# Kernel optimization log

Measured on AMD Instinct MI355X. Metric: run time of the kernel, lower is better.

The kernel has to match this reference:

```python
import jax, jax.numpy as jnp
import numpy as np

# ArcFace hyperparameters (match init_kwargs)
M1 = 1.0
M2 = 0.5
M3 = 0.0
SCALE = 64.0
LS = 0.0  # label_smoothing
THRESHOLD = float(np.cos((np.pi - M2) / M1))  # easy-margin threshold
THETA_MIN = (-1.0 - M3) * 2.0

B, C = 512, 100000


def setup_inputs() -> dict:
    key = jax.random.key(0)
    kl, kx = jax.random.split(key)
    labels = jax.random.randint(kl, (B,), 0, C)
    # y_true is a one-hot target matrix, as implied by `torch.where(y_true != 0)` picking one entry per row
    y_true = jax.nn.one_hot(labels, C, dtype=jnp.float32)
    # norm_logits are cosine similarities in (-1, 1); keep away from endpoints so acos is well-conditioned
    norm_logits = jax.random.uniform(kx, (B, C), jnp.float32, -0.99, 0.99)
    return {"y_true": y_true, "norm_logits": norm_logits}


def reference(y_true, norm_logits):
    b, c = norm_logits.shape
    labels = jnp.argmax(y_true, axis=-1)           # [B] index of the single nonzero per row
    rows = jnp.arange(b)
    vals = norm_logits[rows, labels]               # gather cos(theta) at true-label positions
    # margin1 == 1.0 and margin3 == 0.0 -> theta = cos(acos(x) + m2) branch
    theta = jnp.cos(jnp.arccos(vals) * M1 + M2) - M3
    theta_valid = jnp.where(vals > THRESHOLD, theta, THETA_MIN - theta)
    arcface_logits = norm_logits.at[rows, labels].set(theta_valid) * SCALE
    log_p = jax.nn.log_softmax(arcface_logits, axis=-1)
    # F.cross_entropy with probability targets + label smoothing
    target = y_true * (1.0 - LS) + LS / c
    return -jnp.mean(jnp.sum(target * log_p, axis=-1))
```

## Files before the change

kernel.cpp:

```cpp
#include <hip/hip_runtime.h>
#include <math.h>


#define BB 512
#define CC 100000
#define C4 (CC / 4)
#define BLK 1024

#define K64 92.33248261689366f

typedef unsigned int u32x4 __attribute__((ext_vector_type(4)));
typedef float f32x4 __attribute__((ext_vector_type(4)));

__device__ __forceinline__ float wave_reduce_add(float v) {
    #pragma unroll
    for (int off = 32; off > 0; off >>= 1)
        v += __shfl_down(v, off, 64);
    return v;
}

__device__ __forceinline__ float e64(float x) {
    return __builtin_amdgcn_exp2f(fmaf(K64, x, -K64));
}

__global__ __launch_bounds__(BLK) void arcface_rows(const float* __restrict__ y_true,
                                                    const float* __restrict__ logits,
                                                    float* __restrict__ row_loss) {
    const int row = blockIdx.x;
    const int tid = threadIdx.x;
    const u32x4* __restrict__ y4 = (const u32x4*)(y_true + (size_t)row * CC);
    const f32x4* __restrict__ x4 = (const f32x4*)(logits + (size_t)row * CC);

    __shared__ int s_lab;
    __shared__ float s_sum[BLK / 64];

    #pragma unroll 1
    for (int i = tid; i < C4; i += BLK) {
        const u32x4 u = __builtin_nontemporal_load(&y4[i]);
        if (u.x | u.y | u.z | u.w) {
            const int off = u.x ? 0 : (u.y ? 1 : (u.z ? 2 : 3));
            s_lab = 4 * i + off;
        }
    }
    __syncthreads();

    float val = 0.0f;
    if (tid == 0) val = logits[(size_t)row * CC + s_lab];

    float s0 = 0.0f, s1 = 0.0f;
    #pragma unroll 1
    for (int i = tid; i < C4; i += BLK) {
        const f32x4 x = x4[i];
        s0 += e64(x.x); s1 += e64(x.y); s0 += e64(x.z); s1 += e64(x.w);
    }

    float s = wave_reduce_add(s0 + s1);
    if ((tid & 63) == 0) s_sum[tid >> 6] = s;
    __syncthreads();

    if (tid == 0) {
        float total = 0.0f;
        #pragma unroll
        for (int w = 0; w < BLK / 64; ++w) total += s_sum[w];

        const float THRESH = -0.8775825618903728f;
        const float theta = cosf(acosf(val) + 0.5f);
        const float tv = (val > THRESH) ? theta : (-2.0f - theta);

        total += e64(tv) - e64(val);

        row_loss[row] = 64.0f + logf(total) - 64.0f * tv;
    }
}

__global__ __launch_bounds__(BB) void reduce_rows(const float* __restrict__ row_loss,
                                                  float* __restrict__ out) {
    const int tid = threadIdx.x;
    float v = row_loss[tid];
    v = wave_reduce_add(v);
    __shared__ float s_wave[BB / 64];
    if ((tid & 63) == 0) s_wave[tid >> 6] = v;
    __syncthreads();
    if (tid == 0) {
        float t = 0.0f;
        #pragma unroll
        for (int w = 0; w < BB / 64; ++w) t += s_wave[w];
        out[0] = t * (1.0f / (float)BB);
    }
}

extern "C" void kernel_launch(void* const* d_in, const int* in_sizes, int n_in,
                              void* d_out, int out_size, void* d_ws, size_t ws_size,
                              hipStream_t stream) {
    const float* y_true = (const float*)d_in[0];
    const float* logits = (const float*)d_in[1];
    float* out = (float*)d_out;
    float* row_loss = (float*)d_ws;

    arcface_rows<<<BB, BLK, 0, stream>>>(y_true, logits, row_loss);
    reduce_rows<<<1, BB, 0, stream>>>(row_loss, out);
}
```

Before: 64.30 us.

## Stop one-hot scan early and fuse final mean via atomicAdd

Threads scanning a row of the one-hot matrix now check a shared volatile flag and stop as soon as any thread in the block has found the label, which skips the remaining y_true reads for that row. The separate reduction kernel is replaced by a memset of the output plus an atomicAdd of each row's scaled loss. The early exit only helps when the label lies early in a thread's stride, because every thread still reads its first chunk. The atomic accumulation makes the summation order nondeterministic.

```diff
diff --git a/kernel.cpp b/kernel.cpp
--- a/kernel.cpp
+++ b/kernel.cpp
@@ -25,7 +25,7 @@
 
 __global__ __launch_bounds__(BLK) void arcface_rows(const float* __restrict__ y_true,
                                                     const float* __restrict__ logits,
-                                                    float* __restrict__ row_loss) {
+                                                    float* __restrict__ out) {
     const int row = blockIdx.x;
     const int tid = threadIdx.x;
     const u32x4* __restrict__ y4 = (const u32x4*)(y_true + (size_t)row * CC);
@@ -34,18 +34,24 @@
     __shared__ int s_lab;
     __shared__ float s_sum[BLK / 64];
 
+    if (tid == 0) s_lab = -1;
+    __syncthreads();
+    volatile int* vlab = &s_lab;
+
     #pragma unroll 1
     for (int i = tid; i < C4; i += BLK) {
+        if (*vlab >= 0) break;
         const u32x4 u = __builtin_nontemporal_load(&y4[i]);
         if (u.x | u.y | u.z | u.w) {
             const int off = u.x ? 0 : (u.y ? 1 : (u.z ? 2 : 3));
-            s_lab = 4 * i + off;
+            *vlab = 4 * i + off;
         }
     }
     __syncthreads();
+    const int lab = s_lab;
 
     float val = 0.0f;
-    if (tid == 0) val = logits[(size_t)row * CC + s_lab];
+    if (tid == 0) val = logits[(size_t)row * CC + lab];
 
     float s0 = 0.0f, s1 = 0.0f;
     #pragma unroll 1
@@ -69,23 +75,8 @@
 
         total += e64(tv) - e64(val);
 
-        row_loss[row] = 64.0f + logf(total) - 64.0f * tv;
-    }
-}
-
-__global__ __launch_bounds__(BB) void reduce_rows(const float* __restrict__ row_loss,
-                                                  float* __restrict__ out) {
-    const int tid = threadIdx.x;
-    float v = row_loss[tid];
-    v = wave_reduce_add(v);
-    __shared__ float s_wave[BB / 64];
-    if ((tid & 63) == 0) s_wave[tid >> 6] = v;
-    __syncthreads();
-    if (tid == 0) {
-        float t = 0.0f;
-        #pragma unroll
-        for (int w = 0; w < BB / 64; ++w) t += s_wave[w];
-        out[0] = t * (1.0f / (float)BB);
+        const float loss = 64.0f + logf(total) - 64.0f * tv;
+        atomicAdd(out, loss * (1.0f / (float)BB));
     }
 }
 
@@ -95,8 +86,7 @@
     const float* y_true = (const float*)d_in[0];
     const float* logits = (const float*)d_in[1];
     float* out = (float*)d_out;
-    float* row_loss = (float*)d_ws;
 
-    arcface_rows<<<BB, BLK, 0, stream>>>(y_true, logits, row_loss);
-    reduce_rows<<<1, BB, 0, stream>>>(row_loss, out);
+    hipMemsetAsync(out, 0, sizeof(float), stream);
+    arcface_rows<<<BB, BLK, 0, stream>>>(y_true, logits, out);
 }
```

Result: faster. 55.53 us (-13.6%).

## Split label search and exp-sum into separate blocks with early-exit label scan

Applied to the files above, without the earlier changes.

Each row now gets two blocks. One block only scans the one-hot row to find the label, and it stops scanning once a shared volatile flag shows the label was found. The other block only computes the scaled exp-sum over the logits. The final log and mean are moved into the combine kernel, which reads three per-row workspace arrays. This removes the serial dependency between the two scans, doubles the block count, and on average avoids reading about half of y_true. The cost is extra workspace traffic and a volatile shared-memory poll on every loop iteration.

```diff
diff --git a/kernel.cpp b/kernel.cpp
--- a/kernel.cpp
+++ b/kernel.cpp
@@ -23,60 +23,70 @@
     return __builtin_amdgcn_exp2f(fmaf(K64, x, -K64));
 }
 
-__global__ __launch_bounds__(BLK) void arcface_rows(const float* __restrict__ y_true,
+__global__ __launch_bounds__(BLK) void arcface_main(const float* __restrict__ y_true,
                                                     const float* __restrict__ logits,
-                                                    float* __restrict__ row_loss) {
-    const int row = blockIdx.x;
+                                                    float* __restrict__ ws_total,
+                                                    float* __restrict__ ws_corr,
+                                                    float* __restrict__ ws_tv) {
+    const int row = blockIdx.x >> 1;
     const int tid = threadIdx.x;
-    const u32x4* __restrict__ y4 = (const u32x4*)(y_true + (size_t)row * CC);
-    const f32x4* __restrict__ x4 = (const f32x4*)(logits + (size_t)row * CC);
 
-    __shared__ int s_lab;
-    __shared__ float s_sum[BLK / 64];
+    if (blockIdx.x & 1) {
+        const u32x4* __restrict__ y4 = (const u32x4*)(y_true + (size_t)row * CC);
+        __shared__ int s_lab;
+        if (tid == 0) s_lab = -1;
+        __syncthreads();
+        volatile int* vlab = &s_lab;
 
-    #pragma unroll 1
-    for (int i = tid; i < C4; i += BLK) {
-        const u32x4 u = __builtin_nontemporal_load(&y4[i]);
-        if (u.x | u.y | u.z | u.w) {
-            const int off = u.x ? 0 : (u.y ? 1 : (u.z ? 2 : 3));
-            s_lab = 4 * i + off;
+        #pragma unroll 1
+        for (int i = tid; i < C4; i += BLK) {
+            if (*vlab >= 0) break;
+            const u32x4 u = __builtin_nontemporal_load(&y4[i]);
+            if (u.x | u.y | u.z | u.w) {
+                const int off = u.x ? 0 : (u.y ? 1 : (u.z ? 2 : 3));
+                *vlab = 4 * i + off;
+            }
         }
-    }
-    __syncthreads();
+        __syncthreads();
 
-    float val = 0.0f;
-    if (tid == 0) val = logits[(size_t)row * CC + s_lab];
+        if (tid == 0) {
+            const float val = logits[(size_t)row * CC + s_lab];
+            const float THRESH = -0.8775825618903728f;
+            const float theta = cosf(acosf(val) + 0.5f);
+            const float tv = (val > THRESH) ? theta : (-2.0f - theta);
+            ws_corr[row] = e64(tv) - e64(val);
+            ws_tv[row] = tv;
+        }
+    } else {
+        const f32x4* __restrict__ x4 = (const f32x4*)(logits + (size_t)row * CC);
+        __shared__ float s_sum[BLK / 64];
 
-    float s0 = 0.0f, s1 = 0.0f;
-    #pragma unroll 1
-    for (int i = tid; i < C4; i += BLK) {
-        const f32x4 x = x4[i];
-        s0 += e64(x.x); s1 += e64(x.y); s0 += e64(x.z); s1 += e64(x.w);
-    }
+        float s0 = 0.0f, s1 = 0.0f;
+        #pragma unroll 1
+        for (int i = tid; i < C4; i += BLK) {
+            const f32x4 x = x4[i];
+            s0 += e64(x.x); s1 += e64(x.y); s0 += e64(x.z); s1 += e64(x.w);
+        }
 
-    float s = wave_reduce_add(s0 + s1);
-    if ((tid & 63) == 0) s_sum[tid >> 6] = s;
-    __syncthreads();
-
-    if (tid == 0) {
-        float total = 0.0f;
-        #pragma unroll
-        for (int w = 0; w < BLK / 64; ++w) total += s_sum[w];
-
-        const float THRESH = -0.8775825618903728f;
-        const float theta = cosf(acosf(val) + 0.5f);
-        const float tv = (val > THRESH) ? theta : (-2.0f - theta);
-
-        total += e64(tv) - e64(val);
-
-        row_loss[row] = 64.0f + logf(total) - 64.0f * tv;
+        float s = wave_reduce_add(s0 + s1);
+        if ((tid & 63) == 0) s_sum[tid >> 6] = s;
+        __syncthreads();
+        if (tid == 0) {
+            float total = 0.0f;
+            #pragma unroll
+            for (int w = 0; w < BLK / 64; ++w) total += s_sum[w];
+            ws_total[row] = total;
+        }
     }
 }
 
-__global__ __launch_bounds__(BB) void reduce_rows(const float* __restrict__ row_loss,
-                                                  float* __restrict__ out) {
+__global__ __launch_bounds__(BB) void combine_rows(const float* __restrict__ ws_total,
+                                                   const float* __restrict__ ws_corr,
+                                                   const float* __restrict__ ws_tv,
+                                                   float* __restrict__ out) {
     const int tid = threadIdx.x;
-    float v = row_loss[tid];
+    const float tv = ws_tv[tid];
+    float v = 64.0f + logf(ws_total[tid] + ws_corr[tid]) - 64.0f * tv;
     v = wave_reduce_add(v);
     __shared__ float s_wave[BB / 64];
     if ((tid & 63) == 0) s_wave[tid >> 6] = v;
@@ -95,8 +105,10 @@
     const float* y_true = (const float*)d_in[0];
     const float* logits = (const float*)d_in[1];
     float* out = (float*)d_out;
-    float* row_loss = (float*)d_ws;
+    float* ws_total = (float*)d_ws;
+    float* ws_corr = ws_total + BB;
+    float* ws_tv = ws_corr + BB;
 
-    arcface_rows<<<BB, BLK, 0, stream>>>(y_true, logits, row_loss);
-    reduce_rows<<<1, BB, 0, stream>>>(row_loss, out);
+    arcface_main<<<2 * BB, BLK, 0, stream>>>(y_true, logits, ws_total, ws_corr, ws_tv);
+    combine_rows<<<1, BB, 0, stream>>>(ws_total, ws_corr, ws_tv, out);
 }
```

After: 51.46 us. 20.0% less time.
